# Performance work log

Measured on AMD Instinct MI355X. Metric: run time of the kernel, lower is better.

The kernel has to match this reference:

```python
import jax, jax.numpy as jnp
import numpy as np

N_NODES = 50000
N_EDGES = 800000
IN_F = 128
OUT_F = 128
HEADS = 8
HEAD_DIM = OUT_F // HEADS
EDGE_F = 64


def setup_inputs() -> dict:
    key = jax.random.key(0)
    ks = jax.random.split(key, 12)
    s = 0.05
    return {
        "node_features": jax.random.normal(ks[0], (N_NODES, IN_F), jnp.float32),
        "edge_index": jax.random.randint(ks[1], (2, N_EDGES), 0, N_NODES, jnp.int32),
        "edge_features": jax.random.normal(ks[2], (N_EDGES, EDGE_F), jnp.float32),
        "Wq": jax.random.normal(ks[3], (IN_F, OUT_F), jnp.float32) * s,
        "bq": jnp.zeros((OUT_F,), jnp.float32),
        "Wk": jax.random.normal(ks[4], (IN_F, OUT_F), jnp.float32) * s,
        "bk": jnp.zeros((OUT_F,), jnp.float32),
        "Wv": jax.random.normal(ks[5], (IN_F, OUT_F), jnp.float32) * s,
        "bv": jnp.zeros((OUT_F,), jnp.float32),
        "We": jax.random.normal(ks[6], (EDGE_F, HEADS), jnp.float32) * s,
        "be": jnp.zeros((HEADS,), jnp.float32),
        "Wo": jax.random.normal(ks[7], (OUT_F, OUT_F), jnp.float32) * s,
        "bo": jnp.zeros((OUT_F,), jnp.float32),
    }


def reference(node_features, edge_index, edge_features,
              Wq, bq, Wk, bk, Wv, bv, We, be, Wo, bo):
    n_nodes = node_features.shape[0]
    scale = HEAD_DIM ** (-0.5)
    sources = edge_index[0]
    targets = edge_index[1]

    q = (node_features @ Wq + bq).reshape(n_nodes, HEADS, HEAD_DIM)
    k = (node_features @ Wk + bk).reshape(n_nodes, HEADS, HEAD_DIM)
    v = (node_features @ Wv + bv).reshape(n_nodes, HEADS, HEAD_DIM)

    # edge-wise gathers: [E, H, D]
    q_t = q[targets]
    k_s = k[sources]
    v_s = v[sources]

    # scores [E, H] with edge bias
    scores = jnp.sum(q_t * k_s, axis=-1) * scale + (edge_features @ We + be)

    # segment softmax over edges sharing a target node
    max_s = jax.ops.segment_max(scores, targets, num_segments=n_nodes)
    e = jnp.exp(scores - max_s[targets])
    denom = jax.ops.segment_sum(e, targets, num_segments=n_nodes) + 1e-10
    probs = e / denom[targets]

    weighted = (probs[:, :, None] * v_s).reshape(scores.shape[0], -1)  # [E, H*D]
    agg = jax.ops.segment_sum(weighted, targets, num_segments=n_nodes)  # [N, H*D]
    return agg @ Wo + bo
```

## Files before the change

kernel.cpp:

```cpp
#include <hip/hip_runtime.h>
#include <hip/hip_bf16.h>
#include <math.h>

#define IN_F   128
#define OUT_F  128
#define HEADS  8
#define HEAD_D 16
#define EDGE_F 64
#define BUCKET 64

typedef __attribute__((ext_vector_type(8))) short bf16x8;
typedef __attribute__((ext_vector_type(4))) float f32x4;

__device__ inline unsigned int f2bf(float f) {
    union { float f; unsigned int u; } c; c.f = f;
    unsigned int r = c.u + 0x7FFFu + ((c.u >> 16) & 1u);
    return r >> 16;
}

__global__ __launch_bounds__(256)
void wprep_kernel(const float* __restrict__ Wq, const float* __restrict__ Wk,
                  const float* __restrict__ Wv, const float* __restrict__ Wo,
                  uint4* __restrict__ Wb) {
    int id = blockIdx.x * 256 + threadIdx.x;
    if (id >= 8192) return;
    int lane = id & 63;
    int kb   = (id >> 6) & 3;
    int ct   = (id >> 8) & 7;
    int mat  = id >> 11;
    const float* W = (mat == 0) ? Wq : (mat == 1) ? Wk : (mat == 2) ? Wv : Wo;
    int n  = ct * 16 + (lane & 15);
    int k0 = kb * 32 + (lane >> 4) * 8;
    unsigned int t[8];
    #pragma unroll
    for (int j = 0; j < 8; ++j) t[j] = f2bf(W[(size_t)(k0 + j) * 128 + n]);
    uint4 val;
    val.x = t[0] | (t[1] << 16);
    val.y = t[2] | (t[3] << 16);
    val.z = t[4] | (t[5] << 16);
    val.w = t[6] | (t[7] << 16);
    Wb[id] = val;
}

__global__ __launch_bounds__(256)
void qkv_mfma(const float* __restrict__ x, const bf16x8* __restrict__ WbV,
              const float* __restrict__ bq, const float* __restrict__ bk,
              const float* __restrict__ bv,
              float* __restrict__ q, unsigned int* __restrict__ kvp, int n_nodes) {
    const int tid  = threadIdx.x;
    const int wave = tid >> 6;
    const int lane = tid & 63;
    const int quad = lane >> 4;
    const int lcol = lane & 15;
    const int row0 = blockIdx.x * 64 + wave * 16;
    const int m    = row0 + lcol;

    bf16x8 afrag[4];
    const bool mv = (m < n_nodes);
    const float* xr = x + (size_t)m * IN_F;
    #pragma unroll
    for (int kb = 0; kb < 4; ++kb) {
        float buf[8];
        if (mv) {
            float4 a = ((const float4*)(xr + kb * 32 + quad * 8))[0];
            float4 b = ((const float4*)(xr + kb * 32 + quad * 8 + 4))[0];
            buf[0]=a.x; buf[1]=a.y; buf[2]=a.z; buf[3]=a.w;
            buf[4]=b.x; buf[5]=b.y; buf[6]=b.z; buf[7]=b.w;
        } else {
            #pragma unroll
            for (int j = 0; j < 8; ++j) buf[j] = 0.f;
        }
        bf16x8 f;
        #pragma unroll
        for (int j = 0; j < 8; ++j) f[j] = (short)f2bf(buf[j]);
        afrag[kb] = f;
    }

    #pragma unroll
    for (int ct = 0; ct < 8; ++ct) {
        f32x4 aq = {0.f,0.f,0.f,0.f}, ak = {0.f,0.f,0.f,0.f}, av = {0.f,0.f,0.f,0.f};
        #pragma unroll
        for (int kb = 0; kb < 4; ++kb) {
            bf16x8 bq_ = WbV[((0 * 8 + ct) * 4 + kb) * 64 + lane];
            bf16x8 bk_ = WbV[((1 * 8 + ct) * 4 + kb) * 64 + lane];
            bf16x8 bv_ = WbV[((2 * 8 + ct) * 4 + kb) * 64 + lane];
            aq = __builtin_amdgcn_mfma_f32_16x16x32_bf16(afrag[kb], bq_, aq, 0, 0, 0);
            ak = __builtin_amdgcn_mfma_f32_16x16x32_bf16(afrag[kb], bk_, ak, 0, 0, 0);
            av = __builtin_amdgcn_mfma_f32_16x16x32_bf16(afrag[kb], bv_, av, 0, 0, 0);
        }
        const int col = ct * 16 + lcol;
        float bqc = bq[col], bkc = bk[col], bvc = bv[col];
        #pragma unroll
        for (int r = 0; r < 4; ++r) {
            int node = row0 + quad * 4 + r;
            if (node < n_nodes) {
                size_t o = (size_t)node * OUT_F + col;
                q[o]   = aq[r] + bqc;
                kvp[o] = f2bf(ak[r] + bkc) | (f2bf(av[r] + bvc) << 16);
            }
        }
    }
}

__global__ __launch_bounds__(256)
void ebias_kernel(const float* __restrict__ ef,
                  const float* __restrict__ We, const float* __restrict__ be,
                  float* __restrict__ ebias, int n_edges) {
    __shared__ float sWe[EDGE_F * HEADS];
    __shared__ float sbe[HEADS];
    const int tid = threadIdx.x;
    for (int i = tid; i < EDGE_F * HEADS; i += 256) sWe[i] = We[i];
    if (tid < HEADS) sbe[tid] = be[tid];
    __syncthreads();

    const int e = blockIdx.x * 256 + tid;
    if (e >= n_edges) return;

    float acc[HEADS];
    #pragma unroll
    for (int h = 0; h < HEADS; ++h) acc[h] = sbe[h];

    const float4* er = (const float4*)(ef + (size_t)e * EDGE_F);
    #pragma unroll
    for (int j4 = 0; j4 < EDGE_F / 4; ++j4) {
        float4 evv = er[j4];
        float ev[4] = {evv.x, evv.y, evv.z, evv.w};
        #pragma unroll
        for (int jj = 0; jj < 4; ++jj) {
            int j = j4 * 4 + jj;
            #pragma unroll
            for (int h = 0; h < HEADS; ++h)
                acc[h] = fmaf(ev[jj], sWe[j * HEADS + h], acc[h]);
        }
    }
    float4* dst = (float4*)(ebias + (size_t)e * HEADS);
    dst[0] = make_float4(acc[0], acc[1], acc[2], acc[3]);
    dst[1] = make_float4(acc[4], acc[5], acc[6], acc[7]);
}

__global__ __launch_bounds__(256)
void scatter_kernel(const int* __restrict__ ei, int* __restrict__ deg,
                    int2* __restrict__ csr2, int n_edges) {
    int e = blockIdx.x * 256 + threadIdx.x;
    if (e < n_edges) {
        int s = ei[e];
        int t = ei[n_edges + e];
        int pos = atomicAdd(&deg[t], 1);
        if (pos < BUCKET) csr2[((size_t)t << 6) + pos] = make_int2(s, e);
    }
}

__global__ __launch_bounds__(128)
void agg_kernel(const int2* __restrict__ csr2, const int* __restrict__ deg,
                const float* __restrict__ q, const unsigned int* __restrict__ kvp,
                const float* __restrict__ ebias, unsigned short* __restrict__ aggn) {
    const int t   = blockIdx.x;
    const int tid = threadIdx.x;
    const int h   = tid >> 4;
    const float qj = q[(size_t)t * OUT_F + tid];

    const int beg = t << 6;
    int cnt = deg[t]; if (cnt > BUCKET) cnt = BUCKET;
    const int end = beg + cnt;

    float acc = 0.f, den = 0.f;

    unsigned int kvw0 = 0, kvw1 = 0;
    float eb0 = 0.f, eb1 = 0.f;
    if (beg < end) {
        int2 se = csr2[beg];
        kvw0 = kvp[(size_t)se.x * OUT_F + tid];
        eb0  = ebias[(size_t)se.y * HEADS + h];
    }
    if (beg + 1 < end) {
        int2 se = csr2[beg + 1];
        kvw1 = kvp[(size_t)se.x * OUT_F + tid];
        eb1  = ebias[(size_t)se.y * HEADS + h];
    }

    int i = beg;
    while (i + 1 < end) {
        unsigned int nkv0 = 0, nkv1 = 0;
        float neb0 = 0.f, neb1 = 0.f;
        if (i + 2 < end) {
            int2 se = csr2[i + 2];
            nkv0 = kvp[(size_t)se.x * OUT_F + tid];
            neb0 = ebias[(size_t)se.y * HEADS + h];
        }
        if (i + 3 < end) {
            int2 se = csr2[i + 3];
            nkv1 = kvp[(size_t)se.x * OUT_F + tid];
            neb1 = ebias[(size_t)se.y * HEADS + h];
        }
        {
            float kf = __uint_as_float(kvw0 << 16);
            float vf = __uint_as_float(kvw0 & 0xFFFF0000u);
            float p = qj * kf;
            p += __shfl_xor(p, 8, 16);
            p += __shfl_xor(p, 4, 16);
            p += __shfl_xor(p, 2, 16);
            p += __shfl_xor(p, 1, 16);
            float w = __expf(fmaf(p, 0.25f, eb0));
            den += w;
            acc = fmaf(w, vf, acc);
        }
        {
            float kf = __uint_as_float(kvw1 << 16);
            float vf = __uint_as_float(kvw1 & 0xFFFF0000u);
            float p = qj * kf;
            p += __shfl_xor(p, 8, 16);
            p += __shfl_xor(p, 4, 16);
            p += __shfl_xor(p, 2, 16);
            p += __shfl_xor(p, 1, 16);
            float w = __expf(fmaf(p, 0.25f, eb1));
            den += w;
            acc = fmaf(w, vf, acc);
        }
        kvw0 = nkv0; eb0 = neb0;
        kvw1 = nkv1; eb1 = neb1;
        i += 2;
    }
    if (i < end) {
        float kf = __uint_as_float(kvw0 << 16);
        float vf = __uint_as_float(kvw0 & 0xFFFF0000u);
        float p = qj * kf;
        p += __shfl_xor(p, 8, 16);
        p += __shfl_xor(p, 4, 16);
        p += __shfl_xor(p, 2, 16);
        p += __shfl_xor(p, 1, 16);
        float w = __expf(fmaf(p, 0.25f, eb0));
        den += w;
        acc = fmaf(w, vf, acc);
    }
    aggn[(size_t)t * OUT_F + tid] = (unsigned short)f2bf(acc / (den + 1e-10f));
}

__global__ __launch_bounds__(256)
void out_mfma(const unsigned short* __restrict__ aggn, const bf16x8* __restrict__ WbV,
              const float* __restrict__ bo, float* __restrict__ out, int n_nodes) {
    const int tid  = threadIdx.x;
    const int wave = tid >> 6;
    const int lane = tid & 63;
    const int quad = lane >> 4;
    const int lcol = lane & 15;
    const int row0 = blockIdx.x * 64 + wave * 16;
    const int m    = row0 + lcol;

    bf16x8 afrag[4];
    const bool mv = (m < n_nodes);
    const bf16x8* ar = (const bf16x8*)(aggn + (size_t)m * OUT_F);
    #pragma unroll
    for (int kb = 0; kb < 4; ++kb) {
        if (mv) afrag[kb] = ar[kb * 4 + quad];
        else {
            bf16x8 z;
            #pragma unroll
            for (int j = 0; j < 8; ++j) z[j] = 0;
            afrag[kb] = z;
        }
    }

    #pragma unroll
    for (int ct = 0; ct < 8; ++ct) {
        f32x4 acc = {0.f, 0.f, 0.f, 0.f};
        #pragma unroll
        for (int kb = 0; kb < 4; ++kb) {
            bf16x8 b = WbV[((3 * 8 + ct) * 4 + kb) * 64 + lane];
            acc = __builtin_amdgcn_mfma_f32_16x16x32_bf16(afrag[kb], b, acc, 0, 0, 0);
        }
        const int col = ct * 16 + lcol;
        float boc = bo[col];
        #pragma unroll
        for (int r = 0; r < 4; ++r) {
            int node = row0 + quad * 4 + r;
            if (node < n_nodes) out[(size_t)node * OUT_F + col] = acc[r] + boc;
        }
    }
}

extern "C" void kernel_launch(void* const* d_in, const int* in_sizes, int n_in,
                              void* d_out, int out_size, void* d_ws, size_t ws_size,
                              hipStream_t stream) {
    const float* x  = (const float*)d_in[0];
    const int*   ei = (const int*)  d_in[1];
    const float* ef = (const float*)d_in[2];
    const float* Wq = (const float*)d_in[3];
    const float* bq = (const float*)d_in[4];
    const float* Wk = (const float*)d_in[5];
    const float* bk = (const float*)d_in[6];
    const float* Wv = (const float*)d_in[7];
    const float* bv = (const float*)d_in[8];
    const float* We = (const float*)d_in[9];
    const float* be = (const float*)d_in[10];
    const float* Wo = (const float*)d_in[11];
    const float* bo = (const float*)d_in[12];
    float* out = (float*)d_out;

    const int n_nodes = in_sizes[0] / IN_F;
    const int n_edges = in_sizes[1] / 2;

    char* w = (char*)d_ws;
    float*          q     = (float*)w;          w += (size_t)n_nodes * OUT_F * 4;
    unsigned int*   kvp   = (unsigned int*)w;   w += (size_t)n_nodes * OUT_F * 4;
    float*          ebias = (float*)w;          w += (size_t)n_edges * HEADS * 4;
    unsigned short* aggn  = (unsigned short*)w; w += (size_t)n_nodes * OUT_F * 2;
    uint4*          Wb    = (uint4*)w;          w += (size_t)8192 * 16;
    int*            deg   = (int*)w;            w += (size_t)n_nodes * 4;
    int2*           csr2  = (int2*)w;

    hipMemsetAsync(deg, 0, (size_t)n_nodes * sizeof(int), stream);

    wprep_kernel<<<32, 256, 0, stream>>>(Wq, Wk, Wv, Wo, Wb);

    qkv_mfma<<<(n_nodes + 63) / 64, 256, 0, stream>>>(
        x, (const bf16x8*)Wb, bq, bk, bv, q, kvp, n_nodes);

    ebias_kernel<<<(n_edges + 255) / 256, 256, 0, stream>>>(ef, We, be, ebias, n_edges);

    scatter_kernel<<<(n_edges + 255) / 256, 256, 0, stream>>>(ei, deg, csr2, n_edges);

    agg_kernel<<<n_nodes, 128, 0, stream>>>(csr2, deg, q, kvp, ebias, aggn);

    out_mfma<<<(n_nodes + 63) / 64, 256, 0, stream>>>(aggn, (const bf16x8*)Wb, bo, out, n_nodes);
}
```

Baseline: 514.7 us.

## Fuse prep kernels and remap aggregation to one wave per node with paired features

Folds the degree memset into the weight-prep kernel and merges the QKV GEMM, edge-bias and CSR scatter kernels into one launch that splits blocks by role. Aggregation now gives each target node a single 64-lane wave. Each lane loads a 64-bit packed K/V pair through a permuted kvp layout, so the dot-product reduction needs fewer shuffles. Edge prefetch is deepened to four slots. This cuts launch count and per-edge shuffle and load overhead, at the cost of more register pressure and a mixed-role fused kernel.

```diff
diff --git a/kernel.cpp b/kernel.cpp
--- a/kernel.cpp
+++ b/kernel.cpp
@@ -18,11 +18,16 @@
     return r >> 16;
 }
 
+__device__ inline int wperm(int col) {
+    return (col & 0x70) | ((col & 7) << 1) | ((col >> 3) & 1);
+}
+
 __global__ __launch_bounds__(256)
-void wprep_kernel(const float* __restrict__ Wq, const float* __restrict__ Wk,
-                  const float* __restrict__ Wv, const float* __restrict__ Wo,
-                  uint4* __restrict__ Wb) {
+void prep_kernel(const float* __restrict__ Wq, const float* __restrict__ Wk,
+                 const float* __restrict__ Wv, const float* __restrict__ Wo,
+                 uint4* __restrict__ Wb, int* __restrict__ deg, int n_nodes) {
     int id = blockIdx.x * 256 + threadIdx.x;
+    if (id < n_nodes) deg[id] = 0;
     if (id >= 8192) return;
     int lane = id & 63;
     int kb   = (id >> 6) & 3;
@@ -43,196 +48,191 @@
 }
 
 __global__ __launch_bounds__(256)
-void qkv_mfma(const float* __restrict__ x, const bf16x8* __restrict__ WbV,
-              const float* __restrict__ bq, const float* __restrict__ bk,
-              const float* __restrict__ bv,
-              float* __restrict__ q, unsigned int* __restrict__ kvp, int n_nodes) {
-    const int tid  = threadIdx.x;
-    const int wave = tid >> 6;
-    const int lane = tid & 63;
-    const int quad = lane >> 4;
-    const int lcol = lane & 15;
-    const int row0 = blockIdx.x * 64 + wave * 16;
-    const int m    = row0 + lcol;
-
-    bf16x8 afrag[4];
-    const bool mv = (m < n_nodes);
-    const float* xr = x + (size_t)m * IN_F;
-    #pragma unroll
-    for (int kb = 0; kb < 4; ++kb) {
-        float buf[8];
-        if (mv) {
-            float4 a = ((const float4*)(xr + kb * 32 + quad * 8))[0];
-            float4 b = ((const float4*)(xr + kb * 32 + quad * 8 + 4))[0];
-            buf[0]=a.x; buf[1]=a.y; buf[2]=a.z; buf[3]=a.w;
-            buf[4]=b.x; buf[5]=b.y; buf[6]=b.z; buf[7]=b.w;
-        } else {
-            #pragma unroll
-            for (int j = 0; j < 8; ++j) buf[j] = 0.f;
-        }
-        bf16x8 f;
-        #pragma unroll
-        for (int j = 0; j < 8; ++j) f[j] = (short)f2bf(buf[j]);
-        afrag[kb] = f;
-    }
-
-    #pragma unroll
-    for (int ct = 0; ct < 8; ++ct) {
-        f32x4 aq = {0.f,0.f,0.f,0.f}, ak = {0.f,0.f,0.f,0.f}, av = {0.f,0.f,0.f,0.f};
-        #pragma unroll
-        for (int kb = 0; kb < 4; ++kb) {
-            bf16x8 bq_ = WbV[((0 * 8 + ct) * 4 + kb) * 64 + lane];
-            bf16x8 bk_ = WbV[((1 * 8 + ct) * 4 + kb) * 64 + lane];
-            bf16x8 bv_ = WbV[((2 * 8 + ct) * 4 + kb) * 64 + lane];
-            aq = __builtin_amdgcn_mfma_f32_16x16x32_bf16(afrag[kb], bq_, aq, 0, 0, 0);
-            ak = __builtin_amdgcn_mfma_f32_16x16x32_bf16(afrag[kb], bk_, ak, 0, 0, 0);
-            av = __builtin_amdgcn_mfma_f32_16x16x32_bf16(afrag[kb], bv_, av, 0, 0, 0);
-        }
-        const int col = ct * 16 + lcol;
-        float bqc = bq[col], bkc = bk[col], bvc = bv[col];
-        #pragma unroll
-        for (int r = 0; r < 4; ++r) {
-            int node = row0 + quad * 4 + r;
-            if (node < n_nodes) {
-                size_t o = (size_t)node * OUT_F + col;
-                q[o]   = aq[r] + bqc;
-                kvp[o] = f2bf(ak[r] + bkc) | (f2bf(av[r] + bvc) << 16);
-            }
-        }
-    }
-}
-
-__global__ __launch_bounds__(256)
-void ebias_kernel(const float* __restrict__ ef,
-                  const float* __restrict__ We, const float* __restrict__ be,
-                  float* __restrict__ ebias, int n_edges) {
+void qkv_edges(const float* __restrict__ x, const bf16x8* __restrict__ WbV,
+               const float* __restrict__ bq, const float* __restrict__ bk,
+               const float* __restrict__ bv,
+               float* __restrict__ q, unsigned int* __restrict__ kvp, int n_nodes,
+               const float* __restrict__ ef, const float* __restrict__ We,
+               const float* __restrict__ be, float* __restrict__ ebias,
+               const int* __restrict__ ei, int* __restrict__ deg,
+               int2* __restrict__ csr2, int n_edges, int node_blocks) {
     __shared__ float sWe[EDGE_F * HEADS];
     __shared__ float sbe[HEADS];
     const int tid = threadIdx.x;
-    for (int i = tid; i < EDGE_F * HEADS; i += 256) sWe[i] = We[i];
-    if (tid < HEADS) sbe[tid] = be[tid];
-    __syncthreads();
-
-    const int e = blockIdx.x * 256 + tid;
-    if (e >= n_edges) return;
-
-    float acc[HEADS];
-    #pragma unroll
-    for (int h = 0; h < HEADS; ++h) acc[h] = sbe[h];
-
-    const float4* er = (const float4*)(ef + (size_t)e * EDGE_F);
-    #pragma unroll
-    for (int j4 = 0; j4 < EDGE_F / 4; ++j4) {
-        float4 evv = er[j4];
-        float ev[4] = {evv.x, evv.y, evv.z, evv.w};
-        #pragma unroll
-        for (int jj = 0; jj < 4; ++jj) {
-            int j = j4 * 4 + jj;
-            #pragma unroll
-            for (int h = 0; h < HEADS; ++h)
-                acc[h] = fmaf(ev[jj], sWe[j * HEADS + h], acc[h]);
-        }
-    }
-    float4* dst = (float4*)(ebias + (size_t)e * HEADS);
-    dst[0] = make_float4(acc[0], acc[1], acc[2], acc[3]);
-    dst[1] = make_float4(acc[4], acc[5], acc[6], acc[7]);
-}
-
-__global__ __launch_bounds__(256)
-void scatter_kernel(const int* __restrict__ ei, int* __restrict__ deg,
-                    int2* __restrict__ csr2, int n_edges) {
-    int e = blockIdx.x * 256 + threadIdx.x;
-    if (e < n_edges) {
+
+    if ((int)blockIdx.x < node_blocks) {
+        const int wave = tid >> 6;
+        const int lane = tid & 63;
+        const int quad = lane >> 4;
+        const int lcol = lane & 15;
+        const int row0 = blockIdx.x * 64 + wave * 16;
+        const int m    = row0 + lcol;
+
+        bf16x8 afrag[4];
+        const bool mv = (m < n_nodes);
+        const float* xr = x + (size_t)m * IN_F;
+        #pragma unroll
+        for (int kb = 0; kb < 4; ++kb) {
+            float buf[8];
+            if (mv) {
+                float4 a = ((const float4*)(xr + kb * 32 + quad * 8))[0];
+                float4 b = ((const float4*)(xr + kb * 32 + quad * 8 + 4))[0];
+                buf[0]=a.x; buf[1]=a.y; buf[2]=a.z; buf[3]=a.w;
+                buf[4]=b.x; buf[5]=b.y; buf[6]=b.z; buf[7]=b.w;
+            } else {
+                #pragma unroll
+                for (int j = 0; j < 8; ++j) buf[j] = 0.f;
+            }
+            bf16x8 f;
+            #pragma unroll
+            for (int j = 0; j < 8; ++j) f[j] = (short)f2bf(buf[j]);
+            afrag[kb] = f;
+        }
+
+        #pragma unroll
+        for (int ct = 0; ct < 8; ++ct) {
+            f32x4 aq = {0.f,0.f,0.f,0.f}, ak = {0.f,0.f,0.f,0.f}, av = {0.f,0.f,0.f,0.f};
+            #pragma unroll
+            for (int kb = 0; kb < 4; ++kb) {
+                bf16x8 bq_ = WbV[((0 * 8 + ct) * 4 + kb) * 64 + lane];
+                bf16x8 bk_ = WbV[((1 * 8 + ct) * 4 + kb) * 64 + lane];
+                bf16x8 bv_ = WbV[((2 * 8 + ct) * 4 + kb) * 64 + lane];
+                aq = __builtin_amdgcn_mfma_f32_16x16x32_bf16(afrag[kb], bq_, aq, 0, 0, 0);
+                ak = __builtin_amdgcn_mfma_f32_16x16x32_bf16(afrag[kb], bk_, ak, 0, 0, 0);
+                av = __builtin_amdgcn_mfma_f32_16x16x32_bf16(afrag[kb], bv_, av, 0, 0, 0);
+            }
+            const int col = ct * 16 + lcol;
+            const int wcol = wperm(col);
+            float bqc = bq[col], bkc = bk[col], bvc = bv[col];
+            #pragma unroll
+            for (int r = 0; r < 4; ++r) {
+                int node = row0 + quad * 4 + r;
+                if (node < n_nodes) {
+                    q[(size_t)node * OUT_F + col]    = aq[r] + bqc;
+                    kvp[(size_t)node * OUT_F + wcol] = f2bf(ak[r] + bkc) | (f2bf(av[r] + bvc) << 16);
+                }
+            }
+        }
+    } else {
+        for (int i = tid; i < EDGE_F * HEADS; i += 256) sWe[i] = We[i];
+        if (tid < HEADS) sbe[tid] = be[tid];
+        __syncthreads();
+
+        const int e = (blockIdx.x - node_blocks) * 256 + tid;
+        if (e >= n_edges) return;
+
         int s = ei[e];
         int t = ei[n_edges + e];
         int pos = atomicAdd(&deg[t], 1);
         if (pos < BUCKET) csr2[((size_t)t << 6) + pos] = make_int2(s, e);
-    }
-}
-
-__global__ __launch_bounds__(128)
+
+        float acc[HEADS];
+        #pragma unroll
+        for (int h = 0; h < HEADS; ++h) acc[h] = sbe[h];
+
+        const float4* er = (const float4*)(ef + (size_t)e * EDGE_F);
+        #pragma unroll
+        for (int j4 = 0; j4 < EDGE_F / 4; ++j4) {
+            float4 evv = er[j4];
+            float ev[4] = {evv.x, evv.y, evv.z, evv.w};
+            #pragma unroll
+            for (int jj = 0; jj < 4; ++jj) {
+                int j = j4 * 4 + jj;
+                #pragma unroll
+                for (int h = 0; h < HEADS; ++h)
+                    acc[h] = fmaf(ev[jj], sWe[j * HEADS + h], acc[h]);
+            }
+        }
+        float4* dst = (float4*)(ebias + (size_t)e * HEADS);
+        dst[0] = make_float4(acc[0], acc[1], acc[2], acc[3]);
+        dst[1] = make_float4(acc[4], acc[5], acc[6], acc[7]);
+    }
+}
+
+__global__ __launch_bounds__(256)
 void agg_kernel(const int2* __restrict__ csr2, const int* __restrict__ deg,
-                const float* __restrict__ q, const unsigned int* __restrict__ kvp,
-                const float* __restrict__ ebias, unsigned short* __restrict__ aggn) {
-    const int t   = blockIdx.x;
-    const int tid = threadIdx.x;
-    const int h   = tid >> 4;
-    const float qj = q[(size_t)t * OUT_F + tid];
+                const float* __restrict__ q, const unsigned long long* __restrict__ kvpu,
+                const float* __restrict__ ebias, unsigned short* __restrict__ aggn,
+                int n_nodes) {
+    const int tid  = threadIdx.x;
+    const int wave = tid >> 6;
+    const int lane = tid & 63;
+    const int t    = blockIdx.x * 4 + wave;
+    if (t >= n_nodes) return;
+
+    const int h  = lane >> 3;
+    const int r  = lane & 7;
+    const int fa = h * 16 + r;
+
+    const float qa = q[(size_t)t * OUT_F + fa];
+    const float qb = q[(size_t)t * OUT_F + fa + 8];
 
     const int beg = t << 6;
     int cnt = deg[t]; if (cnt > BUCKET) cnt = BUCKET;
     const int end = beg + cnt;
 
-    float acc = 0.f, den = 0.f;
-
-    unsigned int kvw0 = 0, kvw1 = 0;
-    float eb0 = 0.f, eb1 = 0.f;
-    if (beg < end) {
-        int2 se = csr2[beg];
-        kvw0 = kvp[(size_t)se.x * OUT_F + tid];
-        eb0  = ebias[(size_t)se.y * HEADS + h];
-    }
-    if (beg + 1 < end) {
-        int2 se = csr2[beg + 1];
-        kvw1 = kvp[(size_t)se.x * OUT_F + tid];
-        eb1  = ebias[(size_t)se.y * HEADS + h];
-    }
+    float acc_a = 0.f, acc_b = 0.f, den = 0.f;
+
+    auto process = [&](unsigned long long kv, float eb) {
+        unsigned int w0 = (unsigned int)kv;
+        unsigned int w1 = (unsigned int)(kv >> 32);
+        float ka = __uint_as_float(w0 << 16);
+        float va = __uint_as_float(w0 & 0xFFFF0000u);
+        float kb = __uint_as_float(w1 << 16);
+        float vb = __uint_as_float(w1 & 0xFFFF0000u);
+        float pa = __fmul_rn(qa, ka);
+        float pb = __fmul_rn(qb, kb);
+        float p  = __fadd_rn(pa, pb);
+        p = __fadd_rn(p, __shfl_xor(p, 4, 8));
+        p = __fadd_rn(p, __shfl_xor(p, 2, 8));
+        p = __fadd_rn(p, __shfl_xor(p, 1, 8));
+        float w = __expf(fmaf(p, 0.25f, eb));
+        den += w;
+        acc_a = fmaf(w, va, acc_a);
+        acc_b = fmaf(w, vb, acc_b);
+    };
+
+    unsigned long long kv0 = 0, kv1 = 0, kv2 = 0, kv3 = 0;
+    float eb0 = 0.f, eb1 = 0.f, eb2 = 0.f, eb3 = 0.f;
+
+    #define LOADSLOT(kvs, ebs, idx)                                          \
+        if ((idx) < end) {                                                   \
+            int2 se = csr2[(idx)];                                           \
+            kvs = kvpu[(size_t)se.x * 64 + lane];                            \
+            ebs = ebias[(size_t)se.y * HEADS + h];                           \
+        }
+
+    LOADSLOT(kv0, eb0, beg)
+    LOADSLOT(kv1, eb1, beg + 1)
+    LOADSLOT(kv2, eb2, beg + 2)
+    LOADSLOT(kv3, eb3, beg + 3)
 
     int i = beg;
-    while (i + 1 < end) {
-        unsigned int nkv0 = 0, nkv1 = 0;
-        float neb0 = 0.f, neb1 = 0.f;
-        if (i + 2 < end) {
-            int2 se = csr2[i + 2];
-            nkv0 = kvp[(size_t)se.x * OUT_F + tid];
-            neb0 = ebias[(size_t)se.y * HEADS + h];
-        }
-        if (i + 3 < end) {
-            int2 se = csr2[i + 3];
-            nkv1 = kvp[(size_t)se.x * OUT_F + tid];
-            neb1 = ebias[(size_t)se.y * HEADS + h];
-        }
-        {
-            float kf = __uint_as_float(kvw0 << 16);
-            float vf = __uint_as_float(kvw0 & 0xFFFF0000u);
-            float p = qj * kf;
-            p += __shfl_xor(p, 8, 16);
-            p += __shfl_xor(p, 4, 16);
-            p += __shfl_xor(p, 2, 16);
-            p += __shfl_xor(p, 1, 16);
-            float w = __expf(fmaf(p, 0.25f, eb0));
-            den += w;
-            acc = fmaf(w, vf, acc);
-        }
-        {
-            float kf = __uint_as_float(kvw1 << 16);
-            float vf = __uint_as_float(kvw1 & 0xFFFF0000u);
-            float p = qj * kf;
-            p += __shfl_xor(p, 8, 16);
-            p += __shfl_xor(p, 4, 16);
-            p += __shfl_xor(p, 2, 16);
-            p += __shfl_xor(p, 1, 16);
-            float w = __expf(fmaf(p, 0.25f, eb1));
-            den += w;
-            acc = fmaf(w, vf, acc);
-        }
-        kvw0 = nkv0; eb0 = neb0;
-        kvw1 = nkv1; eb1 = neb1;
-        i += 2;
-    }
-    if (i < end) {
-        float kf = __uint_as_float(kvw0 << 16);
-        float vf = __uint_as_float(kvw0 & 0xFFFF0000u);
-        float p = qj * kf;
-        p += __shfl_xor(p, 8, 16);
-        p += __shfl_xor(p, 4, 16);
-        p += __shfl_xor(p, 2, 16);
-        p += __shfl_xor(p, 1, 16);
-        float w = __expf(fmaf(p, 0.25f, eb0));
-        den += w;
-        acc = fmaf(w, vf, acc);
-    }
-    aggn[(size_t)t * OUT_F + tid] = (unsigned short)f2bf(acc / (den + 1e-10f));
+    while (i + 3 < end) {
+        unsigned long long n0 = 0, n1 = 0, n2 = 0, n3 = 0;
+        float f0 = 0.f, f1 = 0.f, f2 = 0.f, f3 = 0.f;
+        LOADSLOT(n0, f0, i + 4)
+        LOADSLOT(n1, f1, i + 5)
+        LOADSLOT(n2, f2, i + 6)
+        LOADSLOT(n3, f3, i + 7)
+        process(kv0, eb0);
+        process(kv1, eb1);
+        process(kv2, eb2);
+        process(kv3, eb3);
+        kv0 = n0; eb0 = f0;
+        kv1 = n1; eb1 = f1;
+        kv2 = n2; eb2 = f2;
+        kv3 = n3; eb3 = f3;
+        i += 4;
+    }
+    if (i < end)     process(kv0, eb0);
+    if (i + 1 < end) process(kv1, eb1);
+    if (i + 2 < end) process(kv2, eb2);
+    #undef LOADSLOT
+
+    float d = den + 1e-10f;
+    aggn[(size_t)t * OUT_F + fa]     = (unsigned short)f2bf(acc_a / d);
+    aggn[(size_t)t * OUT_F + fa + 8] = (unsigned short)f2bf(acc_b / d);
 }
 
 __global__ __launch_bounds__(256)
@@ -308,18 +308,23 @@
     int*            deg   = (int*)w;            w += (size_t)n_nodes * 4;
     int2*           csr2  = (int2*)w;
 
-    hipMemsetAsync(deg, 0, (size_t)n_nodes * sizeof(int), stream);
-
-    wprep_kernel<<<32, 256, 0, stream>>>(Wq, Wk, Wv, Wo, Wb);
-
-    qkv_mfma<<<(n_nodes + 63) / 64, 256, 0, stream>>>(
-        x, (const bf16x8*)Wb, bq, bk, bv, q, kvp, n_nodes);
-
-    ebias_kernel<<<(n_edges + 255) / 256, 256, 0, stream>>>(ef, We, be, ebias, n_edges);
-
-    scatter_kernel<<<(n_edges + 255) / 256, 256, 0, stream>>>(ei, deg, csr2, n_edges);
-
-    agg_kernel<<<n_nodes, 128, 0, stream>>>(csr2, deg, q, kvp, ebias, aggn);
-
-    out_mfma<<<(n_nodes + 63) / 64, 256, 0, stream>>>(aggn, (const bf16x8*)Wb, bo, out, n_nodes);
-}
+    {
+        int threads_needed = (n_nodes > 8192) ? n_nodes : 8192;
+        prep_kernel<<<(threads_needed + 255) / 256, 256, 0, stream>>>(
+            Wq, Wk, Wv, Wo, Wb, deg, n_nodes);
+    }
+
+    {
+        int node_blocks = (n_nodes + 63) / 64;
+        int edge_blocks = (n_edges + 255) / 256;
+        qkv_edges<<<node_blocks + edge_blocks, 256, 0, stream>>>(
+            x, (const bf16x8*)Wb, bq, bk, bv, q, kvp, n_nodes,
+            ef, We, be, ebias, ei, deg, csr2, n_edges, node_blocks);
+    }
+
+    agg_kernel<<<(n_nodes + 3) / 4, 256, 0, stream>>>(
+        csr2, deg, q, (const unsigned long long*)kvp, ebias, aggn, n_nodes);
+
+    out_mfma<<<(n_nodes + 63) / 64, 256, 0, stream>>>(
+        aggn, (const bf16x8*)Wb, bo, out, n_nodes);
+}
```

After: 482.5 us. 6.3% less time.
